# Kernel optimization log

Measured on AMD Instinct MI355X. Metric: run time of the kernel, lower is better.

The kernel has to match this reference:

```python
import jax, jax.numpy as jnp
import numpy as np
import math

B, S, D = 2, 512, 768
N_HEADS, HEAD = 12, 64
ALPHA = 32.0


def setup_inputs() -> dict:
    key = jax.random.key(0)
    ks = jax.random.split(key, 12)
    w_scale = 1.0 / math.sqrt(D)
    return {
        "hidden_states": jax.random.normal(ks[0], (B, S, D), jnp.float32),
        "attention_mask": jnp.zeros((B, 1, 1, S), jnp.float32),
        "rel_pos": jax.random.normal(ks[1], (B, S, S, HEAD), jnp.float32),
        "rel_2d_pos": jax.random.normal(ks[2], (B, S, S, HEAD), jnp.float32),
        "rel_2d_angle": jax.random.normal(ks[3], (B, S, S, HEAD), jnp.float32),
        "Wq": jax.random.normal(ks[4], (D, D), jnp.float32) * w_scale,
        "bq": jnp.zeros((D,), jnp.float32),
        "Wk": jax.random.normal(ks[5], (D, D), jnp.float32) * w_scale,
        "bk": jnp.zeros((D,), jnp.float32),
        "Wv": jax.random.normal(ks[6], (D, D), jnp.float32) * w_scale,
        "bv": jnp.zeros((D,), jnp.float32),
    }


def _heads(x):
    # (B,S,D) -> (B,N,S,HEAD)
    b, s, _ = x.shape
    return x.reshape(b, s, N_HEADS, HEAD).transpose(0, 2, 1, 3)


def reference(hidden_states, attention_mask, rel_pos, rel_2d_pos, rel_2d_angle,
              Wq, bq, Wk, bk, Wv, bv):
    q = _heads(hidden_states @ Wq.T + bq)
    k = _heads(hidden_states @ Wk.T + bk)
    v = _heads(hidden_states @ Wv.T + bv)

    qs = q / math.sqrt(HEAD)  # scaled query, (B,N,S,HEAD)
    scores = jnp.einsum('bnsh,bnkh->bnsk', qs, k)
    scores = scores + jnp.einsum('bnsh,bskh->bnsk', qs, rel_pos)
    scores = scores + jnp.einsum('bnsh,bskh->bnsk', qs, rel_2d_pos)
    scores = scores + jnp.einsum('bnsh,bskh->bnsk', qs, rel_2d_angle)
    scores = scores + attention_mask

    # cogview (PB-Relax) softmax: subtract per-row max of scores/alpha, rescale
    scaled = scores / ALPHA
    m = jnp.max(scaled, axis=-1, keepdims=True)
    probs = jax.nn.softmax((scaled - m) * ALPHA, axis=-1)

    ctx = jnp.einsum('bnsk,bnkh->bsnh', probs, v)  # (B,S,N,HEAD)
    return ctx.reshape(ctx.shape[0], ctx.shape[1], N_HEADS * HEAD)
```

## Files before the change

kernel.cpp:

```cpp
#include <hip/hip_runtime.h>

typedef __attribute__((ext_vector_type(8))) short short8;
typedef __attribute__((ext_vector_type(4))) float f32x4;

#define B_ 2
#define S_ 512
#define D_ 768
#define NH 12
#define HD 64

__device__ inline short f2bf(float f) {
    union { float f; unsigned u; } v; v.f = f;
    unsigned r = v.u + 0x7fffu + ((v.u >> 16) & 1u);
    return (short)(r >> 16);
}

__device__ __forceinline__ f32x4 ntload4(const float* p) {
    return __builtin_nontemporal_load((const f32x4*)p);
}

__global__ __launch_bounds__(256) void qkv_gemm(
    const float* __restrict__ hidden,
    const float* __restrict__ Wq, const float* __restrict__ Wk, const float* __restrict__ Wv,
    const float* __restrict__ bq, const float* __restrict__ bk, const float* __restrict__ bv,
    short* __restrict__ qbf, short* __restrict__ kbf, short* __restrict__ vbf)
{
    __shared__ short hs[64 * 72];
    __shared__ short wt[64 * 72];

    const int mt = blockIdx.x, nt = blockIdx.y, mat = blockIdx.z;
    const int m0 = mt * 64, n0 = nt * 64;
    const float* W    = (mat == 0) ? Wq : ((mat == 1) ? Wk : Wv);
    const float* bias = (mat == 0) ? bq : ((mat == 1) ? bk : bv);

    const int tid = threadIdx.x;
    const int w = tid >> 6, l = tid & 63;
    const int sr = tid >> 2, sc = (tid & 3) * 16;

    f32x4 acc[4];
    #pragma unroll
    for (int i = 0; i < 4; ++i) acc[i] = (f32x4){0.f, 0.f, 0.f, 0.f};

    const int arow = (w * 16 + (l & 15)) * 72 + (l >> 4) * 8;

    for (int kt = 0; kt < 12; ++kt) {
        const int d0 = kt * 64;
        if (kt) __syncthreads();
        {
            const float4* sa = (const float4*)(hidden + (size_t)(m0 + sr) * D_ + d0 + sc);
            float4 x0 = sa[0], x1 = sa[1], x2 = sa[2], x3 = sa[3];
            short8 p0 = {f2bf(x0.x), f2bf(x0.y), f2bf(x0.z), f2bf(x0.w),
                         f2bf(x1.x), f2bf(x1.y), f2bf(x1.z), f2bf(x1.w)};
            short8 p1 = {f2bf(x2.x), f2bf(x2.y), f2bf(x2.z), f2bf(x2.w),
                         f2bf(x3.x), f2bf(x3.y), f2bf(x3.z), f2bf(x3.w)};
            *(short8*)&hs[sr * 72 + sc]     = p0;
            *(short8*)&hs[sr * 72 + sc + 8] = p1;
            const float4* sb = (const float4*)(W + (size_t)(n0 + sr) * D_ + d0 + sc);
            float4 y0 = sb[0], y1 = sb[1], y2 = sb[2], y3 = sb[3];
            short8 q0 = {f2bf(y0.x), f2bf(y0.y), f2bf(y0.z), f2bf(y0.w),
                         f2bf(y1.x), f2bf(y1.y), f2bf(y1.z), f2bf(y1.w)};
            short8 q1 = {f2bf(y2.x), f2bf(y2.y), f2bf(y2.z), f2bf(y2.w),
                         f2bf(y3.x), f2bf(y3.y), f2bf(y3.z), f2bf(y3.w)};
            *(short8*)&wt[sr * 72 + sc]     = q0;
            *(short8*)&wt[sr * 72 + sc + 8] = q1;
        }
        __syncthreads();
        short8 a0 = *(const short8*)&hs[arow];
        short8 a1 = *(const short8*)&hs[arow + 32];
        #pragma unroll
        for (int ct = 0; ct < 4; ++ct) {
            const int brow = (ct * 16 + (l & 15)) * 72 + (l >> 4) * 8;
            short8 b0 = *(const short8*)&wt[brow];
            short8 b1 = *(const short8*)&wt[brow + 32];
            acc[ct] = __builtin_amdgcn_mfma_f32_16x16x32_bf16(a0, b0, acc[ct], 0, 0, 0);
            acc[ct] = __builtin_amdgcn_mfma_f32_16x16x32_bf16(a1, b1, acc[ct], 0, 0, 0);
        }
    }

    if (mat == 2) {
        __syncthreads();
        #pragma unroll
        for (int ct = 0; ct < 4; ++ct) {
            #pragma unroll
            for (int rr = 0; rr < 4; ++rr) {
                const int m_l = w * 16 + (l >> 4) * 4 + rr;
                const int n_l = ct * 16 + (l & 15);
                hs[n_l * 68 + m_l] = f2bf(acc[ct][rr] + bias[n0 + n_l]);
            }
        }
        __syncthreads();
        const int b   = m0 >> 9;
        const int s0b = m0 & 511;
        #pragma unroll
        for (int j = 0; j < 2; ++j) {
            const int idx  = j * 256 + tid;
            const int h    = idx >> 3;
            const int sseg = (idx & 7) * 8;
            short8 vv = *(const short8*)&hs[h * 68 + sseg];
            *(short8*)(vbf + ((size_t)(b * NH + nt) * HD + h) * S_ + s0b + sseg) = vv;
        }
    } else {
        #pragma unroll
        for (int ct = 0; ct < 4; ++ct) {
            #pragma unroll
            for (int rr = 0; rr < 4; ++rr) {
                const int m_l = w * 16 + (l >> 4) * 4 + rr;
                const int n_l = ct * 16 + (l & 15);
                const int m = m0 + m_l;
                const int b = m >> 9, s = m & 511;
                float v = acc[ct][rr] + bias[n0 + n_l];
                const size_t dst = (((size_t)(b * NH + nt) * S_) + s) * HD + n_l;
                if (mat == 0) qbf[dst] = f2bf(v * 0.125f);
                else          kbf[dst] = f2bf(v);
            }
        }
    }
}

__global__ __launch_bounds__(256) void score_qk(
    const short* __restrict__ qbf, const short* __restrict__ kbf,
    const float* __restrict__ mask, float* __restrict__ scores)
{
    __shared__ short qa[64 * 72];
    __shared__ short kb[64 * 72];

    const int st = blockIdx.x, ktile = blockIdx.y, z = blockIdx.z;
    const int b = z / NH, n = z % NH;
    const int s0 = st * 64, k0 = ktile * 64;
    const int tid = threadIdx.x;
    const int w = tid >> 6, l = tid & 63;
    const int sr = tid >> 2, sc = (tid & 3) * 16;

    {
        const short8* sa = (const short8*)(qbf + (((size_t)(b * NH + n) * S_) + s0 + sr) * HD + sc);
        *(short8*)&qa[sr * 72 + sc]     = sa[0];
        *(short8*)&qa[sr * 72 + sc + 8] = sa[1];
        const short8* sb = (const short8*)(kbf + (((size_t)(b * NH + n) * S_) + k0 + sr) * HD + sc);
        *(short8*)&kb[sr * 72 + sc]     = sb[0];
        *(short8*)&kb[sr * 72 + sc + 8] = sb[1];
    }
    __syncthreads();

    f32x4 acc[4];
    #pragma unroll
    for (int i = 0; i < 4; ++i) acc[i] = (f32x4){0.f, 0.f, 0.f, 0.f};

    const int arow = (w * 16 + (l & 15)) * 72 + (l >> 4) * 8;
    short8 a0 = *(const short8*)&qa[arow];
    short8 a1 = *(const short8*)&qa[arow + 32];
    #pragma unroll
    for (int ct = 0; ct < 4; ++ct) {
        const int brow = (ct * 16 + (l & 15)) * 72 + (l >> 4) * 8;
        short8 b0 = *(const short8*)&kb[brow];
        short8 b1 = *(const short8*)&kb[brow + 32];
        acc[ct] = __builtin_amdgcn_mfma_f32_16x16x32_bf16(a0, b0, acc[ct], 0, 0, 0);
        acc[ct] = __builtin_amdgcn_mfma_f32_16x16x32_bf16(a1, b1, acc[ct], 0, 0, 0);
    }

    #pragma unroll
    for (int ct = 0; ct < 4; ++ct) {
        const int kcol = k0 + ct * 16 + (l & 15);
        const float mv = mask[b * S_ + kcol];
        #pragma unroll
        for (int rr = 0; rr < 4; ++rr) {
            const int s_l = w * 16 + (l >> 4) * 4 + rr;
            scores[(((size_t)(b * S_ + s0 + s_l)) * NH + n) * S_ + kcol]
                = acc[ct][rr] + mv;
        }
    }
}

__global__ __launch_bounds__(256) void score_rel(
    const short* __restrict__ qbf,
    const float* __restrict__ rel1, const float* __restrict__ rel2, const float* __restrict__ rel3,
    float* __restrict__ scores)
{
    const int kt = blockIdx.x;
    const int s  = blockIdx.y;
    const int b  = blockIdx.z;
    const int tid = threadIdx.x;
    const int w = tid >> 6, l = tid & 63;

    const int rowsel = l & 15;
    const int hc     = (l >> 4) * 8;

    const int kc = kt * 4 + w;
    const size_t rbase = ((size_t)(b * S_ + s)) * S_ * HD;
    const size_t ro = rbase + (size_t)(kc * 16 + rowsel) * HD + hc;

    f32x4 p0a = ntload4(rel1 + ro);
    f32x4 p0b = ntload4(rel1 + ro + 4);
    f32x4 q0a = ntload4(rel1 + ro + 32);
    f32x4 q0b = ntload4(rel1 + ro + 36);
    f32x4 p1a = ntload4(rel2 + ro);
    f32x4 p1b = ntload4(rel2 + ro + 4);
    f32x4 q1a = ntload4(rel2 + ro + 32);
    f32x4 q1b = ntload4(rel2 + ro + 36);
    f32x4 p2a = ntload4(rel3 + ro);
    f32x4 p2b = ntload4(rel3 + ro + 4);
    f32x4 q2a = ntload4(rel3 + ro + 32);
    f32x4 q2b = ntload4(rel3 + ro + 36);

    short8 a0 = {0, 0, 0, 0, 0, 0, 0, 0};
    short8 a1 = {0, 0, 0, 0, 0, 0, 0, 0};
    if (rowsel < NH) {
        const short* qp = qbf + (((size_t)(b * NH + rowsel) * S_) + s) * HD;
        a0 = *(const short8*)(qp + hc);
        a1 = *(const short8*)(qp + hc + 32);
    }

    short8 b0 = {
        f2bf(p0a.x + p1a.x + p2a.x), f2bf(p0a.y + p1a.y + p2a.y),
        f2bf(p0a.z + p1a.z + p2a.z), f2bf(p0a.w + p1a.w + p2a.w),
        f2bf(p0b.x + p1b.x + p2b.x), f2bf(p0b.y + p1b.y + p2b.y),
        f2bf(p0b.z + p1b.z + p2b.z), f2bf(p0b.w + p1b.w + p2b.w)};
    short8 b1 = {
        f2bf(q0a.x + q1a.x + q2a.x), f2bf(q0a.y + q1a.y + q2a.y),
        f2bf(q0a.z + q1a.z + q2a.z), f2bf(q0a.w + q1a.w + q2a.w),
        f2bf(q0b.x + q1b.x + q2b.x), f2bf(q0b.y + q1b.y + q2b.y),
        f2bf(q0b.z + q1b.z + q2b.z), f2bf(q0b.w + q1b.w + q2b.w)};

    f32x4 acc = (f32x4){0.f, 0.f, 0.f, 0.f};
    acc = __builtin_amdgcn_mfma_f32_16x16x32_bf16(a0, b0, acc, 0, 0, 0);
    acc = __builtin_amdgcn_mfma_f32_16x16x32_bf16(a1, b1, acc, 0, 0, 0);

    const int kg = kc * 16 + rowsel;
    #pragma unroll
    for (int rr = 0; rr < 4; ++rr) {
        const int n = (l >> 4) * 4 + rr;
        if (n < NH) {
            float* p = scores + (((size_t)(b * S_ + s)) * NH + n) * S_ + kg;
            *p += acc[rr];
        }
    }
}

__global__ __launch_bounds__(256) void smpv(
    const float* __restrict__ scores, const short* __restrict__ vbf,
    float* __restrict__ out)
{
    __shared__ short pbf[16][524];

    const int st  = blockIdx.x;
    const int n   = blockIdx.y;
    const int b   = blockIdx.z;
    const int s0  = st * 16;
    const int tid = threadIdx.x;
    const int w = tid >> 6, l = tid & 63;

    for (int r = 0; r < 4; ++r) {
        const int row = w * 4 + r;
        const float* sp = scores + (((size_t)(b * S_ + s0 + row)) * NH + n) * S_;
        float vals[8];
        float m = -1e30f;
        #pragma unroll
        for (int i = 0; i < 8; ++i) { vals[i] = sp[l + 64 * i]; m = fmaxf(m, vals[i]); }
        #pragma unroll
        for (int off = 32; off >= 1; off >>= 1) m = fmaxf(m, __shfl_xor(m, off));
        float sum = 0.f;
        #pragma unroll
        for (int i = 0; i < 8; ++i) { vals[i] = __expf(vals[i] - m); sum += vals[i]; }
        #pragma unroll
        for (int off = 32; off >= 1; off >>= 1) sum += __shfl_xor(sum, off);
        const float inv = 1.0f / sum;
        #pragma unroll
        for (int i = 0; i < 8; ++i) pbf[row][l + 64 * i] = f2bf(vals[i] * inv);
    }
    __syncthreads();

    const int arow = l & 15;
    const int g    = l >> 4;
    f32x4 pacc = (f32x4){0.f, 0.f, 0.f, 0.f};
    const short* vrow = vbf + ((size_t)(b * NH + n) * HD + w * 16 + arow) * S_ + g * 8;
    #pragma unroll
    for (int kk = 0; kk < 16; ++kk) {
        short8 aP = *(const short8*)&pbf[arow][kk * 32 + g * 8];
        short8 bV = *(const short8*)(vrow + kk * 32);
        pacc = __builtin_amdgcn_mfma_f32_16x16x32_bf16(aP, bV, pacc, 0, 0, 0);
    }
    #pragma unroll
    for (int rr = 0; rr < 4; ++rr) {
        const int srow = g * 4 + rr;
        out[((size_t)(b * S_ + s0 + srow)) * D_ + n * HD + w * 16 + arow] = pacc[rr];
    }
}

extern "C" void kernel_launch(void* const* d_in, const int* in_sizes, int n_in,
                              void* d_out, int out_size, void* d_ws, size_t ws_size,
                              hipStream_t stream) {
    const float* hidden = (const float*)d_in[0];
    const float* mask   = (const float*)d_in[1];
    const float* rel1   = (const float*)d_in[2];
    const float* rel2   = (const float*)d_in[3];
    const float* rel3   = (const float*)d_in[4];
    const float* Wq     = (const float*)d_in[5];
    const float* bq     = (const float*)d_in[6];
    const float* Wk     = (const float*)d_in[7];
    const float* bk     = (const float*)d_in[8];
    const float* Wv     = (const float*)d_in[9];
    const float* bv     = (const float*)d_in[10];
    float* out = (float*)d_out;

    const size_t per = (size_t)B_ * NH * S_ * HD;
    short* qbf    = (short*)d_ws;
    short* kbf    = qbf + per;
    short* vbf    = kbf + per;
    float* scores = (float*)(vbf + per);

    qkv_gemm<<<dim3(16, 12, 3), 256, 0, stream>>>(hidden, Wq, Wk, Wv, bq, bk, bv, qbf, kbf, vbf);
    score_qk<<<dim3(8, 8, 24), 256, 0, stream>>>(qbf, kbf, mask, scores);
    score_rel<<<dim3(8, S_, B_), 256, 0, stream>>>(qbf, rel1, rel2, rel3, scores);
    smpv<<<dim3(S_ / 16, NH, B_), 256, 0, stream>>>(scores, vbf, out);
}
```

Measured before the change: 134.1 us.

## Merge QK and relative-position score kernels into one launch with separate bf16 rel buffer

Combines the QK score kernel and the relative-position score kernel into a single launch that splits its blocks by index, so the two parts run concurrently. The rel scores go to a separate bf16 buffer instead of a read-modify-write on the fp32 scores, and the softmax kernel adds the two buffers on load. The f2bf helper now calls the library bf16 conversion. This removes one launch, the fp32 read-modify-write traffic and the ordering between the two score passes. In exchange it adds a second buffer that the softmax kernel must read, and the rel contribution is rounded to bf16 before it is summed.

```diff
diff --git a/kernel.cpp b/kernel.cpp
--- a/kernel.cpp
+++ b/kernel.cpp
@@ -1,4 +1,5 @@
 #include <hip/hip_runtime.h>
+#include <hip/hip_bf16.h>
 
 typedef __attribute__((ext_vector_type(8))) short short8;
 typedef __attribute__((ext_vector_type(4))) float f32x4;
@@ -9,10 +10,16 @@
 #define NH 12
 #define HD 64
 
-__device__ inline short f2bf(float f) {
-    union { float f; unsigned u; } v; v.f = f;
-    unsigned r = v.u + 0x7fffu + ((v.u >> 16) & 1u);
-    return (short)(r >> 16);
+__device__ __forceinline__ short f2bf(float f) {
+    union { __hip_bfloat16 h; short s; } u;
+    u.h = __float2bfloat16(f);
+    return u.s;
+}
+
+__device__ __forceinline__ float bf2f(short s) {
+    union { unsigned u; float f; } v;
+    v.u = ((unsigned)(unsigned short)s) << 16;
+    return v.f;
 }
 
 __device__ __forceinline__ f32x4 ntload4(const float* p) {
@@ -117,127 +124,126 @@
     }
 }
 
-__global__ __launch_bounds__(256) void score_qk(
+__global__ __launch_bounds__(256) void relqk(
     const short* __restrict__ qbf, const short* __restrict__ kbf,
-    const float* __restrict__ mask, float* __restrict__ scores)
+    const float* __restrict__ rel1, const float* __restrict__ rel2, const float* __restrict__ rel3,
+    const float* __restrict__ mask,
+    short* __restrict__ relsc, float* __restrict__ qks)
 {
     __shared__ short qa[64 * 72];
     __shared__ short kb[64 * 72];
 
-    const int st = blockIdx.x, ktile = blockIdx.y, z = blockIdx.z;
-    const int b = z / NH, n = z % NH;
-    const int s0 = st * 64, k0 = ktile * 64;
+    const int bid = blockIdx.x;
     const int tid = threadIdx.x;
     const int w = tid >> 6, l = tid & 63;
-    const int sr = tid >> 2, sc = (tid & 3) * 16;
-
-    {
-        const short8* sa = (const short8*)(qbf + (((size_t)(b * NH + n) * S_) + s0 + sr) * HD + sc);
-        *(short8*)&qa[sr * 72 + sc]     = sa[0];
-        *(short8*)&qa[sr * 72 + sc + 8] = sa[1];
-        const short8* sb = (const short8*)(kbf + (((size_t)(b * NH + n) * S_) + k0 + sr) * HD + sc);
-        *(short8*)&kb[sr * 72 + sc]     = sb[0];
-        *(short8*)&kb[sr * 72 + sc + 8] = sb[1];
-    }
-    __syncthreads();
-
-    f32x4 acc[4];
-    #pragma unroll
-    for (int i = 0; i < 4; ++i) acc[i] = (f32x4){0.f, 0.f, 0.f, 0.f};
-
-    const int arow = (w * 16 + (l & 15)) * 72 + (l >> 4) * 8;
-    short8 a0 = *(const short8*)&qa[arow];
-    short8 a1 = *(const short8*)&qa[arow + 32];
-    #pragma unroll
-    for (int ct = 0; ct < 4; ++ct) {
-        const int brow = (ct * 16 + (l & 15)) * 72 + (l >> 4) * 8;
-        short8 b0 = *(const short8*)&kb[brow];
-        short8 b1 = *(const short8*)&kb[brow + 32];
-        acc[ct] = __builtin_amdgcn_mfma_f32_16x16x32_bf16(a0, b0, acc[ct], 0, 0, 0);
-        acc[ct] = __builtin_amdgcn_mfma_f32_16x16x32_bf16(a1, b1, acc[ct], 0, 0, 0);
-    }
-
-    #pragma unroll
-    for (int ct = 0; ct < 4; ++ct) {
-        const int kcol = k0 + ct * 16 + (l & 15);
-        const float mv = mask[b * S_ + kcol];
+
+    if (bid < 8192) {
+        const int kt = bid & 7;
+        const int s  = (bid >> 3) & 511;
+        const int b  = bid >> 12;
+
+        const int rowsel = l & 15;
+        const int hc     = (l >> 4) * 8;
+
+        const int kc = kt * 4 + w;
+        const size_t rbase = ((size_t)(b * S_ + s)) * S_ * HD;
+        const size_t ro = rbase + (size_t)(kc * 16 + rowsel) * HD + hc;
+
+        f32x4 p0a = ntload4(rel1 + ro);
+        f32x4 p0b = ntload4(rel1 + ro + 4);
+        f32x4 q0a = ntload4(rel1 + ro + 32);
+        f32x4 q0b = ntload4(rel1 + ro + 36);
+        f32x4 p1a = ntload4(rel2 + ro);
+        f32x4 p1b = ntload4(rel2 + ro + 4);
+        f32x4 q1a = ntload4(rel2 + ro + 32);
+        f32x4 q1b = ntload4(rel2 + ro + 36);
+        f32x4 p2a = ntload4(rel3 + ro);
+        f32x4 p2b = ntload4(rel3 + ro + 4);
+        f32x4 q2a = ntload4(rel3 + ro + 32);
+        f32x4 q2b = ntload4(rel3 + ro + 36);
+
+        short8 a0 = {0, 0, 0, 0, 0, 0, 0, 0};
+        short8 a1 = {0, 0, 0, 0, 0, 0, 0, 0};
+        if (rowsel < NH) {
+            const short* qp = qbf + (((size_t)(b * NH + rowsel) * S_) + s) * HD;
+            a0 = *(const short8*)(qp + hc);
+            a1 = *(const short8*)(qp + hc + 32);
+        }
+
+        short8 b0 = {
+            f2bf(p0a.x + p1a.x + p2a.x), f2bf(p0a.y + p1a.y + p2a.y),
+            f2bf(p0a.z + p1a.z + p2a.z), f2bf(p0a.w + p1a.w + p2a.w),
+            f2bf(p0b.x + p1b.x + p2b.x), f2bf(p0b.y + p1b.y + p2b.y),
+            f2bf(p0b.z + p1b.z + p2b.z), f2bf(p0b.w + p1b.w + p2b.w)};
+        short8 b1 = {
+            f2bf(q0a.x + q1a.x + q2a.x), f2bf(q0a.y + q1a.y + q2a.y),
+            f2bf(q0a.z + q1a.z + q2a.z), f2bf(q0a.w + q1a.w + q2a.w),
+            f2bf(q0b.x + q1b.x + q2b.x), f2bf(q0b.y + q1b.y + q2b.y),
+            f2bf(q0b.z + q1b.z + q2b.z), f2bf(q0b.w + q1b.w + q2b.w)};
+
+        f32x4 acc = (f32x4){0.f, 0.f, 0.f, 0.f};
+        acc = __builtin_amdgcn_mfma_f32_16x16x32_bf16(a0, b0, acc, 0, 0, 0);
+        acc = __builtin_amdgcn_mfma_f32_16x16x32_bf16(a1, b1, acc, 0, 0, 0);
+
+        const int kg = kc * 16 + rowsel;
         #pragma unroll
         for (int rr = 0; rr < 4; ++rr) {
-            const int s_l = w * 16 + (l >> 4) * 4 + rr;
-            scores[(((size_t)(b * S_ + s0 + s_l)) * NH + n) * S_ + kcol]
-                = acc[ct][rr] + mv;
-        }
-    }
-}
-
-__global__ __launch_bounds__(256) void score_rel(
-    const short* __restrict__ qbf,
-    const float* __restrict__ rel1, const float* __restrict__ rel2, const float* __restrict__ rel3,
-    float* __restrict__ scores)
-{
-    const int kt = blockIdx.x;
-    const int s  = blockIdx.y;
-    const int b  = blockIdx.z;
-    const int tid = threadIdx.x;
-    const int w = tid >> 6, l = tid & 63;
-
-    const int rowsel = l & 15;
-    const int hc     = (l >> 4) * 8;
-
-    const int kc = kt * 4 + w;
-    const size_t rbase = ((size_t)(b * S_ + s)) * S_ * HD;
-    const size_t ro = rbase + (size_t)(kc * 16 + rowsel) * HD + hc;
-
-    f32x4 p0a = ntload4(rel1 + ro);
-    f32x4 p0b = ntload4(rel1 + ro + 4);
-    f32x4 q0a = ntload4(rel1 + ro + 32);
-    f32x4 q0b = ntload4(rel1 + ro + 36);
-    f32x4 p1a = ntload4(rel2 + ro);
-    f32x4 p1b = ntload4(rel2 + ro + 4);
-    f32x4 q1a = ntload4(rel2 + ro + 32);
-    f32x4 q1b = ntload4(rel2 + ro + 36);
-    f32x4 p2a = ntload4(rel3 + ro);
-    f32x4 p2b = ntload4(rel3 + ro + 4);
-    f32x4 q2a = ntload4(rel3 + ro + 32);
-    f32x4 q2b = ntload4(rel3 + ro + 36);
-
-    short8 a0 = {0, 0, 0, 0, 0, 0, 0, 0};
-    short8 a1 = {0, 0, 0, 0, 0, 0, 0, 0};
-    if (rowsel < NH) {
-        const short* qp = qbf + (((size_t)(b * NH + rowsel) * S_) + s) * HD;
-        a0 = *(const short8*)(qp + hc);
-        a1 = *(const short8*)(qp + hc + 32);
-    }
-
-    short8 b0 = {
-        f2bf(p0a.x + p1a.x + p2a.x), f2bf(p0a.y + p1a.y + p2a.y),
-        f2bf(p0a.z + p1a.z + p2a.z), f2bf(p0a.w + p1a.w + p2a.w),
-        f2bf(p0b.x + p1b.x + p2b.x), f2bf(p0b.y + p1b.y + p2b.y),
-        f2bf(p0b.z + p1b.z + p2b.z), f2bf(p0b.w + p1b.w + p2b.w)};
-    short8 b1 = {
-        f2bf(q0a.x + q1a.x + q2a.x), f2bf(q0a.y + q1a.y + q2a.y),
-        f2bf(q0a.z + q1a.z + q2a.z), f2bf(q0a.w + q1a.w + q2a.w),
-        f2bf(q0b.x + q1b.x + q2b.x), f2bf(q0b.y + q1b.y + q2b.y),
-        f2bf(q0b.z + q1b.z + q2b.z), f2bf(q0b.w + q1b.w + q2b.w)};
-
-    f32x4 acc = (f32x4){0.f, 0.f, 0.f, 0.f};
-    acc = __builtin_amdgcn_mfma_f32_16x16x32_bf16(a0, b0, acc, 0, 0, 0);
-    acc = __builtin_amdgcn_mfma_f32_16x16x32_bf16(a1, b1, acc, 0, 0, 0);
-
-    const int kg = kc * 16 + rowsel;
-    #pragma unroll
-    for (int rr = 0; rr < 4; ++rr) {
-        const int n = (l >> 4) * 4 + rr;
-        if (n < NH) {
-            float* p = scores + (((size_t)(b * S_ + s)) * NH + n) * S_ + kg;
-            *p += acc[rr];
+            const int n = (l >> 4) * 4 + rr;
+            if (n < NH)
+                relsc[(((size_t)(b * S_ + s)) * NH + n) * S_ + kg] = f2bf(acc[rr]);
+        }
+    } else {
+        const int j     = bid - 8192;
+        const int st    = j & 7;
+        const int ktile = (j >> 3) & 7;
+        const int z     = j >> 6;
+        const int b = z / NH, n = z % NH;
+        const int s0 = st * 64, k0 = ktile * 64;
+        const int sr = tid >> 2, sc = (tid & 3) * 16;
+
+        {
+            const short8* sa = (const short8*)(qbf + (((size_t)(b * NH + n) * S_) + s0 + sr) * HD + sc);
+            *(short8*)&qa[sr * 72 + sc]     = sa[0];
+            *(short8*)&qa[sr * 72 + sc + 8] = sa[1];
+            const short8* sb = (const short8*)(kbf + (((size_t)(b * NH + n) * S_) + k0 + sr) * HD + sc);
+            *(short8*)&kb[sr * 72 + sc]     = sb[0];
+            *(short8*)&kb[sr * 72 + sc + 8] = sb[1];
+        }
+        __syncthreads();
+
+        f32x4 acc[4];
+        #pragma unroll
+        for (int i = 0; i < 4; ++i) acc[i] = (f32x4){0.f, 0.f, 0.f, 0.f};
+
+        const int arow = (w * 16 + (l & 15)) * 72 + (l >> 4) * 8;
+        short8 a0 = *(const short8*)&qa[arow];
+        short8 a1 = *(const short8*)&qa[arow + 32];
+        #pragma unroll
+        for (int ct = 0; ct < 4; ++ct) {
+            const int brow = (ct * 16 + (l & 15)) * 72 + (l >> 4) * 8;
+            short8 b0 = *(const short8*)&kb[brow];
+            short8 b1 = *(const short8*)&kb[brow + 32];
+            acc[ct] = __builtin_amdgcn_mfma_f32_16x16x32_bf16(a0, b0, acc[ct], 0, 0, 0);
+            acc[ct] = __builtin_amdgcn_mfma_f32_16x16x32_bf16(a1, b1, acc[ct], 0, 0, 0);
+        }
+
+        #pragma unroll
+        for (int ct = 0; ct < 4; ++ct) {
+            const int kcol = k0 + ct * 16 + (l & 15);
+            const float mv = mask[b * S_ + kcol];
+            #pragma unroll
+            for (int rr = 0; rr < 4; ++rr) {
+                const int s_l = w * 16 + (l >> 4) * 4 + rr;
+                qks[(((size_t)(b * S_ + s0 + s_l)) * NH + n) * S_ + kcol]
+                    = acc[ct][rr] + mv;
+            }
         }
     }
 }
 
 __global__ __launch_bounds__(256) void smpv(
-    const float* __restrict__ scores, const short* __restrict__ vbf,
-    float* __restrict__ out)
+    const float* __restrict__ qks, const short* __restrict__ relsc,
+    const short* __restrict__ vbf, float* __restrict__ out)
 {
     __shared__ short pbf[16][524];
 
@@ -250,18 +256,23 @@
 
     for (int r = 0; r < 4; ++r) {
         const int row = w * 4 + r;
-        const float* sp = scores + (((size_t)(b * S_ + s0 + row)) * NH + n) * S_;
+        const size_t off = (((size_t)(b * S_ + s0 + row)) * NH + n) * S_;
+        const float* sp = qks + off;
+        const short* rp = relsc + off;
         float vals[8];
         float m = -1e30f;
         #pragma unroll
-        for (int i = 0; i < 8; ++i) { vals[i] = sp[l + 64 * i]; m = fmaxf(m, vals[i]); }
-        #pragma unroll
-        for (int off = 32; off >= 1; off >>= 1) m = fmaxf(m, __shfl_xor(m, off));
+        for (int i = 0; i < 8; ++i) {
+            vals[i] = sp[l + 64 * i] + bf2f(rp[l + 64 * i]);
+            m = fmaxf(m, vals[i]);
+        }
+        #pragma unroll
+        for (int off2 = 32; off2 >= 1; off2 >>= 1) m = fmaxf(m, __shfl_xor(m, off2));
         float sum = 0.f;
         #pragma unroll
         for (int i = 0; i < 8; ++i) { vals[i] = __expf(vals[i] - m); sum += vals[i]; }
         #pragma unroll
-        for (int off = 32; off >= 1; off >>= 1) sum += __shfl_xor(sum, off);
+        for (int off2 = 32; off2 >= 1; off2 >>= 1) sum += __shfl_xor(sum, off2);
         const float inv = 1.0f / sum;
         #pragma unroll
         for (int i = 0; i < 8; ++i) pbf[row][l + 64 * i] = f2bf(vals[i] * inv);
@@ -302,13 +313,14 @@
     float* out = (float*)d_out;
 
     const size_t per = (size_t)B_ * NH * S_ * HD;
-    short* qbf    = (short*)d_ws;
-    short* kbf    = qbf + per;
-    short* vbf    = kbf + per;
-    float* scores = (float*)(vbf + per);
+    const size_t nsk = (size_t)B_ * S_ * NH * S_;
+    short* qbf   = (short*)d_ws;
+    short* kbf   = qbf + per;
+    short* vbf   = kbf + per;
+    short* relsc = vbf + per;
+    float* qks   = (float*)(relsc + nsk);
 
     qkv_gemm<<<dim3(16, 12, 3), 256, 0, stream>>>(hidden, Wq, Wk, Wv, bq, bk, bv, qbf, kbf, vbf);
-    score_qk<<<dim3(8, 8, 24), 256, 0, stream>>>(qbf, kbf, mask, scores);
-    score_rel<<<dim3(8, S_, B_), 256, 0, stream>>>(qbf, rel1, rel2, rel3, scores);
-    smpv<<<dim3(S_ / 16, NH, B_), 256, 0, stream>>>(scores, vbf, out);
-}
+    relqk<<<dim3(8192 + 1536), 256, 0, stream>>>(qbf, kbf, rel1, rel2, rel3, mask, relsc, qks);
+    smpv<<<dim3(S_ / 16, NH, B_), 256, 0, stream>>>(qks, relsc, vbf, out);
+}
```

Result: no change. 134.1 us (+0.1%).
